# Kernel tuning notes

Hardware: AMD Instinct MI355X
Metric: run time of the kernel (lower is better)

Reference implementation:

```python
import jax, jax.numpy as jnp
import numpy as np

EPS = 1e-5
ABIT = 8
WBIT = 8


def ste_round(x):
    # straight-through rounding (HAWQ SymmetricQuantFunction)
    return x + jax.lax.stop_gradient(jnp.round(x) - x)


def quant_act(x, bit=ABIT):
    # per-tensor symmetric activation quantization (QuantAct)
    n = 2.0 ** (bit - 1) - 1  # 127
    scale = jnp.max(jnp.abs(x)) / n
    x_int = jnp.clip(ste_round(x / scale), -n - 1, n)
    return x_int * scale, scale


def setup_inputs() -> dict:
    key = jax.random.key(0)
    k = jax.random.split(key, 6)
    B, C_in, H, W, C_out = 32, 512, 32, 32, 128
    x = jax.random.normal(k[0], (B, C_in, H, W), jnp.float32)
    # incoming activation scale (input assumed already 8-bit quantized)
    act_scaling_factor = (jnp.max(jnp.abs(x)) / 127.0).reshape(1)
    bn_gamma = jax.random.uniform(k[1], (C_in,), jnp.float32, 0.5, 1.5)
    bn_beta = jax.random.normal(k[2], (C_in,), jnp.float32) * 0.1
    bn_mean = jax.random.normal(k[3], (C_in,), jnp.float32) * 0.1
    bn_var = jax.random.uniform(k[4], (C_in,), jnp.float32, 0.5, 1.5)
    conv_weight = jax.random.normal(k[5], (C_out, C_in, 3, 3), jnp.float32) / np.sqrt(C_in * 9)
    return {"x": x, "act_scaling_factor": act_scaling_factor,
            "bn_gamma": bn_gamma, "bn_beta": bn_beta,
            "bn_mean": bn_mean, "bn_var": bn_var,
            "conv_weight": conv_weight}


def reference(x, act_scaling_factor, bn_gamma, bn_beta, bn_mean, bn_var, conv_weight):
    nw = 2.0 ** (WBIT - 1) - 1  # 127
    s_in = act_scaling_factor.reshape(())

    # ---- QuantBn: fold BN into per-channel affine, quantize weight/bias ----
    w_bn = bn_gamma / jnp.sqrt(bn_var + EPS)            # [C_in]
    b_bn = bn_beta - bn_mean * w_bn                      # [C_in]
    ws_bn = jnp.max(jnp.abs(w_bn)) / nw                  # per-tensor weight scale
    w_int = jnp.clip(ste_round(w_bn / ws_bn), -nw - 1, nw)
    bn_sf = ws_bn * s_in                                 # bn output scaling factor
    b_int = ste_round(b_bn / bn_sf)
    x_int = x / s_in
    x = (x_int * w_int[None, :, None, None] + b_int[None, :, None, None]) * bn_sf

    # ---- ReLU ----
    x = jax.nn.relu(x)

    # ---- QuantAct: requantize activations to 8 bit ----
    x, s_act = quant_act(x)

    # ---- QuantConv2d: per-output-channel 8-bit weight quant, int conv ----
    ws_c = jnp.max(jnp.abs(conv_weight), axis=(1, 2, 3)) / nw       # [C_out]
    w_cint = jnp.clip(ste_round(conv_weight / ws_c[:, None, None, None]), -nw - 1, nw)
    y_int = jax.lax.conv_general_dilated(
        x / s_act, w_cint, window_strides=(1, 1), padding=((1, 1), (1, 1)),
        dimension_numbers=("NCHW", "OIHW", "NCHW"))
    conv_sf = s_act * ws_c                               # [C_out]
    y = y_int * conv_sf[None, :, None, None]

    # ---- QuantAct output requant ----
    y, s_out = quant_act(y)
    return (y, s_out)
```

## Files before the change

### kernel.cpp

```cpp
#include <hip/hip_runtime.h>


typedef int v4i __attribute__((ext_vector_type(4)));

#define WS_A1    64
#define WS_B1    2112
#define WS_WSC   4160
#define WS_XMX   4672
#define WS_XMN   6720
#define WS_WQ    8768
#define WS_X2    598592
#define WS_ZROW  18424384

__device__ __forceinline__ float wave_max(float m) {
#pragma unroll
    for (int off = 32; off; off >>= 1) m = fmaxf(m, __shfl_xor(m, off));
    return m;
}

__device__ __forceinline__ void stage16(const char* g, char* s, int lane) {
#if defined(__has_builtin) && __has_builtin(__builtin_amdgcn_global_load_lds)
    __builtin_amdgcn_global_load_lds(
        (const __attribute__((address_space(1))) void*)g,
        (__attribute__((address_space(3))) void*)s, 16, 0, 0);
#else
    *(v4i*)(s + lane * 16) = *(const v4i*)g;
#endif
}

__global__ __launch_bounds__(512) void k_prep(
    const float* __restrict__ gamma, const float* __restrict__ beta,
    const float* __restrict__ mean,  const float* __restrict__ var,
    const float* __restrict__ asf,   const float* __restrict__ cw,
    const float4* __restrict__ x4,
    float* ws_f, unsigned* ws_u, float* __restrict__ wsc,
    signed char* __restrict__ wq) {
    int t = threadIdx.x;
    int bid = blockIdx.x;
    __shared__ float red[16];
    if (bid < 512) {
        int c = bid;
        float mx = -3.4e38f, mn = 3.4e38f;
#pragma unroll
        for (int r = 0; r < 16; ++r) {
            int bbb = r * 2 + (t >> 8);
            float4 v = x4[((size_t)(bbb * 512 + c)) * 256 + (t & 255)];
            mx = fmaxf(mx, fmaxf(fmaxf(v.x, v.y), fmaxf(v.z, v.w)));
            mn = fminf(mn, fminf(fminf(v.x, v.y), fminf(v.z, v.w)));
        }
        mx = wave_max(mx);
        mn = -wave_max(-mn);
        if ((t & 63) == 0) { red[t >> 6] = mx; red[8 + (t >> 6)] = mn; }
        __syncthreads();
        if (t == 0) {
            float M = red[0], N = red[8];
#pragma unroll
            for (int i = 1; i < 8; ++i) { M = fmaxf(M, red[i]); N = fminf(N, red[8 + i]); }
            ws_f[WS_XMX / 4 + c] = M;
            ws_f[WS_XMN / 4 + c] = N;
        }
    } else if (bid < 640) {
        int co = bid - 512;
        const float* w = cw + (size_t)co * 4608;
        float m = 0.f;
        for (int j = t; j < 4608; j += 512) m = fmaxf(m, fabsf(w[j]));
        m = wave_max(m);
        if ((t & 63) == 0) red[t >> 6] = m;
        __syncthreads();
        float mall = red[0];
#pragma unroll
        for (int i = 1; i < 8; ++i) mall = fmaxf(mall, red[i]);
        float sc = mall / 127.0f;
        if (t == 0) wsc[co] = sc;
        int ci = t >> 6, cq = (t >> 4) & 3, cb = t & 15;
#pragma unroll
        for (int tap = 0; tap < 9; ++tap) {
            float q = fminf(fmaxf(rintf(w[t * 9 + tap] / sc), -128.f), 127.f);
            wq[(((size_t)(tap * 8 + ci) * 4 + cq) * 128 + co) * 16 + cb] = (signed char)q;
        }
    } else {
        float wbn = gamma[t] / sqrtf(var[t] + 1e-5f);
        float bbn = beta[t] - mean[t] * wbn;
        float m = wave_max(fabsf(wbn));
        if ((t & 63) == 0) red[t >> 6] = m;
        __syncthreads();
        float mall = red[0];
#pragma unroll
        for (int i = 1; i < 8; ++i) mall = fmaxf(mall, red[i]);
        float ws_bn = mall / 127.0f;
        float s_in  = asf[0];
        float bn_sf = ws_bn * s_in;
        float wint  = fminf(fmaxf(rintf(wbn / ws_bn), -128.f), 127.f);
        float bint  = rintf(bbn / bn_sf);
        ws_f[WS_A1 / 4 + t] = wint * bn_sf / s_in;
        ws_f[WS_B1 / 4 + t] = bint * bn_sf;
        if (t == 0) ws_u[1] = 0u;
    }
}

__global__ __launch_bounds__(256) void k_xquant(
    const float4* __restrict__ x4, float* __restrict__ ws_f,
    unsigned* __restrict__ x2u, unsigned* __restrict__ zrowu) {
    int bb = 31 - (blockIdx.x >> 5), h = blockIdx.x & 31;
    const float* A1 = ws_f + WS_A1 / 4;
    const float* B1 = ws_f + WS_B1 / 4;
    const float* XMX = ws_f + WS_XMX / 4;
    const float* XMN = ws_f + WS_XMN / 4;
    int t = threadIdx.x;

    __shared__ float sred[4];
    float cand = 0.f;
#pragma unroll
    for (int c0 = 0; c0 < 512; c0 += 256) {
        int c = c0 + t;
        float A = A1[c], B = B1[c];
        cand = fmaxf(cand, fmaxf(fmaf(XMX[c], A, B), fmaf(XMN[c], A, B)));
    }
    cand = wave_max(cand);
    if ((t & 63) == 0) sred[t >> 6] = cand;
    __syncthreads();
    float xm = fmaxf(fmaxf(sred[0], sred[1]), fmaxf(sred[2], sred[3]));
    float inv_sact = 127.0f / xm;
    if (blockIdx.x == 0 && t == 0) ws_f[3] = xm / 127.0f;

    size_t rowd = (size_t)(bb * 32 + h) * 4352;
    {
        int p = t >> 3, side = (t >> 2) & 1, d = t & 3;
        x2u[rowd + (p * 34 + side * 33) * 4 + d] = 0u;
    }
    if (blockIdx.x < 17) {
        int idx = blockIdx.x * 256 + t;
        if (idx < 4352) zrowu[idx] = 0u;
    }

    __shared__ unsigned lds[512 * 9];

#pragma unroll
    for (int it = 0; it < 16; ++it) {
        int idx = it * 256 + t;
        int c = idx >> 3, f4 = idx & 7;
        float4 v = x4[((size_t)bb * 512 + c) * 256 + h * 8 + f4];
        float A = A1[c] * inv_sact, B = B1[c] * inv_sact;
        unsigned q0 = (unsigned)(int)fminf(rintf(fmaxf(fmaf(v.x, A, B), 0.f)), 127.f);
        unsigned q1 = (unsigned)(int)fminf(rintf(fmaxf(fmaf(v.y, A, B), 0.f)), 127.f);
        unsigned q2 = (unsigned)(int)fminf(rintf(fmaxf(fmaf(v.z, A, B), 0.f)), 127.f);
        unsigned q3 = (unsigned)(int)fminf(rintf(fmaxf(fmaf(v.w, A, B), 0.f)), 127.f);
        lds[c * 9 + f4] = q0 | (q1 << 8) | (q2 << 16) | (q3 << 24);
    }
    __syncthreads();

#pragma unroll
    for (int it = 0; it < 4; ++it) {
        int p = it * 8 + (t >> 5);
        int s = (t >> 2) & 7;
        int k = t & 3;
        unsigned L[16];
#pragma unroll
        for (int j = 0; j < 16; ++j) L[j] = lds[(p * 16 + j) * 9 + s];
        uint4 o;
        unsigned* op = (unsigned*)&o;
#pragma unroll
        for (int d = 0; d < 4; ++d)
            op[d] = ((L[4 * d] >> (8 * k)) & 255u) |
                    (((L[4 * d + 1] >> (8 * k)) & 255u) << 8) |
                    (((L[4 * d + 2] >> (8 * k)) & 255u) << 16) |
                    (((L[4 * d + 3] >> (8 * k)) & 255u) << 24);
        *(uint4*)(x2u + rowd + (size_t)(p * 34 + s * 4 + 1 + k) * 4) = o;
    }
}

__global__ __launch_bounds__(256, 2) void k_conv(
    const unsigned char* __restrict__ x2, const unsigned char* __restrict__ zrow,
    const signed char* __restrict__ wq,
    const float* __restrict__ wsc, const float* __restrict__ ws_f,
    unsigned* __restrict__ amaxy, float* __restrict__ y) {
    __shared__ char ldsb[73728];
    int t = threadIdx.x;
    int lane = t & 63, wv = t >> 6;
    int kv = wv & 1, rp = wv >> 1;
    int m = lane & 15, quad = lane >> 4;

    int bid = blockIdx.x;
    int tile = (bid & 7) * 64 + (bid >> 3);
    int ch = tile & 1;
    int rg = (tile >> 1) & 7;
    int bb = tile >> 4;
    int co0 = ch * 64;
    int h0 = rg * 4 + rp * 2;

    const unsigned char* xb = x2 + (size_t)bb * (32 * 17408);
    const v4i* rpt[4];
#pragma unroll
    for (int j = 0; j < 4; ++j) {
        int row = h0 - 1 + j;
        rpt[j] = (const v4i*)(((unsigned)row < 32u) ? (xb + (size_t)row * 17408) : zrow);
    }

    v4i acc[4][4];
#pragma unroll
    for (int i = 0; i < 4; ++i)
#pragma unroll
        for (int j = 0; j < 4; ++j) acc[i][j] = (v4i){0, 0, 0, 0};

    int abase = quad * 34 + m;

    for (int j = 0; j < 4; ++j) {
#pragma unroll
        for (int i = 0; i < 18; ++i) {
            int c = wv * 18 + i;
            int kvs = (c >= 36) ? 1 : 0;
            int rem = c - kvs * 36;
            int tap = rem >> 2, cq = rem & 3;
            int ci = kvs * 4 + j;
            const char* g = (const char*)wq +
                ((((size_t)(tap * 8 + ci) * 4 + cq) * 128 + co0) * 16) + lane * 16;
            char* s = ldsb + (((kvs * 9 + tap) * 4 + cq) << 10);
            stage16(g, s, lane);
        }
        __syncthreads();

        int ci = kv * 4 + j;
        const v4i* bbase = (const v4i*)ldsb + kv * 2304;
#pragma unroll
        for (int kh = 0; kh < 3; ++kh)
#pragma unroll
            for (int kw = 0; kw < 3; ++kw) {
                int tap = kh * 3 + kw;
                v4i a[4];
#pragma unroll
                for (int mt = 0; mt < 4; ++mt)
                    a[mt] = rpt[kh + (mt >> 1)][ci * 136 + abase + kw + (mt & 1) * 16];
#pragma unroll
                for (int nt = 0; nt < 4; ++nt) {
                    v4i bf = bbase[(tap * 4 + quad) * 64 + nt * 16 + m];
#pragma unroll
                    for (int mt = 0; mt < 4; ++mt)
                        acc[mt][nt] = __builtin_amdgcn_mfma_i32_16x16x64_i8(a[mt], bf, acc[mt][nt], 0, 0, 0);
                }
            }
        __syncthreads();
    }

    v4i* red = (v4i*)ldsb;
    if (kv == 1) {
#pragma unroll
        for (int mt = 0; mt < 4; ++mt)
#pragma unroll
            for (int nt = 0; nt < 4; ++nt)
                red[((rp * 16 + mt * 4 + nt) << 6) + lane] = acc[mt][nt];
    }
    __syncthreads();
    if (kv == 0) {
#pragma unroll
        for (int mt = 0; mt < 4; ++mt)
#pragma unroll
            for (int nt = 0; nt < 4; ++nt) {
                v4i p = red[((rp * 16 + mt * 4 + nt) << 6) + lane];
                acc[mt][nt].x += p.x; acc[mt][nt].y += p.y;
                acc[mt][nt].z += p.z; acc[mt][nt].w += p.w;
            }

        float s_act = ws_f[3];
        float mx = 0.f;
#pragma unroll
        for (int nt = 0; nt < 4; ++nt) {
            int co = co0 + nt * 16 + m;
            float sf = s_act * wsc[co];
#pragma unroll
            for (int mt = 0; mt < 4; ++mt) {
                int row = h0 + (mt >> 1);
                float* yb = y + ((size_t)(bb * 128 + co)) * 1024 + row * 32 + (mt & 1) * 16;
                float4 vv;
                vv.x = (float)acc[mt][nt][0] * sf;
                vv.y = (float)acc[mt][nt][1] * sf;
                vv.z = (float)acc[mt][nt][2] * sf;
                vv.w = (float)acc[mt][nt][3] * sf;
                *(float4*)(yb + quad * 4) = vv;
                mx = fmaxf(mx, fmaxf(fmaxf(fabsf(vv.x), fabsf(vv.y)),
                                     fmaxf(fabsf(vv.z), fabsf(vv.w))));
            }
        }
        mx = wave_max(mx);
        if (lane == 0) atomicMax(amaxy, __float_as_uint(mx));
    }
}

__global__ __launch_bounds__(256) void k_yquant(float* __restrict__ yout,
                                                const unsigned* __restrict__ ws_u) {
    float s_out = __uint_as_float(ws_u[1]) / 127.0f;
    float4* y4 = (float4*)yout;
    int stride = gridDim.x * blockDim.x;
    for (int i = blockIdx.x * blockDim.x + threadIdx.x; i < 1048576; i += stride) {
        float4 v = y4[i];
        v.x = fminf(fmaxf(rintf(v.x / s_out), -128.f), 127.f) * s_out;
        v.y = fminf(fmaxf(rintf(v.y / s_out), -128.f), 127.f) * s_out;
        v.z = fminf(fmaxf(rintf(v.z / s_out), -128.f), 127.f) * s_out;
        v.w = fminf(fmaxf(rintf(v.w / s_out), -128.f), 127.f) * s_out;
        y4[i] = v;
    }
    if (blockIdx.x == 0 && threadIdx.x == 0) yout[4194304] = s_out;
}

extern "C" void kernel_launch(void* const* d_in, const int* in_sizes, int n_in,
                              void* d_out, int out_size, void* d_ws, size_t ws_size,
                              hipStream_t stream) {
    const float* x     = (const float*)d_in[0];
    const float* asf   = (const float*)d_in[1];
    const float* gamma = (const float*)d_in[2];
    const float* beta  = (const float*)d_in[3];
    const float* mean  = (const float*)d_in[4];
    const float* var   = (const float*)d_in[5];
    const float* cw    = (const float*)d_in[6];

    float*    ws_f = (float*)d_ws;
    unsigned* ws_u = (unsigned*)d_ws;
    signed char*   wq   = (signed char*)d_ws + WS_WQ;
    unsigned char* x2   = (unsigned char*)d_ws + WS_X2;
    unsigned char* zrow = (unsigned char*)d_ws + WS_ZROW;
    float* y = (float*)d_out;

    k_prep<<<641, 512, 0, stream>>>(gamma, beta, mean, var, asf, cw,
                                    (const float4*)x, ws_f, ws_u,
                                    ws_f + WS_WSC / 4, wq);
    k_xquant<<<1024, 256, 0, stream>>>((const float4*)x, ws_f,
                                       (unsigned*)x2, (unsigned*)zrow);
    k_conv<<<512, 256, 0, stream>>>(x2, zrow, wq, ws_f + WS_WSC / 4,
                                    ws_f, ws_u + 1, y);
    k_yquant<<<1024, 256, 0, stream>>>(y, ws_u);
}
```

Measured before the change: 160.2 us.

## Switch conv to 32x32x32 int8 MFMA with halved weight staging and higher occupancy

The int8 conv kernel moves from 16x16x64 MFMA tiles to 32x32x32 tiles. The quantized weight layout changes to match, and per-stage weight staging is halved by iterating over 8 channel chunks instead of 4, so LDS per block drops enough to allow 4 blocks per CU. A-fragment loads are reused across the three kh taps, which cuts global/L2 reads of activation rows. The trade-off is more K-loop iterations with more barriers, plus higher register pressure from the 16-wide accumulators under the tighter launch bound.

```diff
diff --git a/kernel.cpp b/kernel.cpp
--- a/kernel.cpp
+++ b/kernel.cpp
@@ -1,7 +1,8 @@
 #include <hip/hip_runtime.h>
 
 
-typedef int v4i __attribute__((ext_vector_type(4)));
+typedef int v4i  __attribute__((ext_vector_type(4)));
+typedef int v16i __attribute__((ext_vector_type(16)));
 
 #define WS_A1    64
 #define WS_B1    2112
@@ -72,11 +73,11 @@
         for (int i = 1; i < 8; ++i) mall = fmaxf(mall, red[i]);
         float sc = mall / 127.0f;
         if (t == 0) wsc[co] = sc;
-        int ci = t >> 6, cq = (t >> 4) & 3, cb = t & 15;
+        int cdw = t >> 4, cb = t & 15;
 #pragma unroll
         for (int tap = 0; tap < 9; ++tap) {
             float q = fminf(fmaxf(rintf(w[t * 9 + tap] / sc), -128.f), 127.f);
-            wq[(((size_t)(tap * 8 + ci) * 4 + cq) * 128 + co) * 16 + cb] = (signed char)q;
+            wq[(((size_t)tap * 32 + cdw) * 128 + co) * 16 + cb] = (signed char)q;
         }
     } else {
         float wbn = gamma[t] / sqrtf(var[t] + 1e-5f);
@@ -169,16 +170,16 @@
     }
 }
 
-__global__ __launch_bounds__(256, 2) void k_conv(
+__global__ __launch_bounds__(256, 4) void k_conv(
     const unsigned char* __restrict__ x2, const unsigned char* __restrict__ zrow,
     const signed char* __restrict__ wq,
     const float* __restrict__ wsc, const float* __restrict__ ws_f,
     unsigned* __restrict__ amaxy, float* __restrict__ y) {
-    __shared__ char ldsb[73728];
+    __shared__ char ldsb[36864];
     int t = threadIdx.x;
     int lane = t & 63, wv = t >> 6;
     int kv = wv & 1, rp = wv >> 1;
-    int m = lane & 15, quad = lane >> 4;
+    int m = lane & 31, khalf = lane >> 5;
 
     int bid = blockIdx.x;
     int tile = (bid & 7) * 64 + (bid >> 3);
@@ -189,95 +190,96 @@
     int h0 = rg * 4 + rp * 2;
 
     const unsigned char* xb = x2 + (size_t)bb * (32 * 17408);
-    const v4i* rpt[4];
+    const char* rpt[4];
 #pragma unroll
     for (int j = 0; j < 4; ++j) {
         int row = h0 - 1 + j;
-        rpt[j] = (const v4i*)(((unsigned)row < 32u) ? (xb + (size_t)row * 17408) : zrow);
-    }
-
-    v4i acc[4][4];
-#pragma unroll
-    for (int i = 0; i < 4; ++i)
-#pragma unroll
-        for (int j = 0; j < 4; ++j) acc[i][j] = (v4i){0, 0, 0, 0};
-
-    int abase = quad * 34 + m;
-
-    for (int j = 0; j < 4; ++j) {
-#pragma unroll
-        for (int i = 0; i < 18; ++i) {
-            int c = wv * 18 + i;
-            int kvs = (c >= 36) ? 1 : 0;
-            int rem = c - kvs * 36;
-            int tap = rem >> 2, cq = rem & 3;
-            int ci = kvs * 4 + j;
+        rpt[j] = (const char*)(((unsigned)row < 32u) ? (xb + (size_t)row * 17408) : zrow);
+    }
+
+    v16i acc[2][2];
+#pragma unroll
+    for (int i = 0; i < 2; ++i)
+#pragma unroll
+        for (int j = 0; j < 2; ++j)
+#pragma unroll
+            for (int e = 0; e < 16; ++e) acc[i][j][e] = 0;
+
+    for (int j = 0; j < 8; ++j) {
+#pragma unroll
+        for (int i = 0; i < 9; ++i) {
+            int c = wv * 9 + i;
+            int s = (c >= 18) ? 1 : 0;
+            int r = c - s * 18;
+            int tap = r >> 1, kh = r & 1;
+            int ci = s * 8 + j;
             const char* g = (const char*)wq +
-                ((((size_t)(tap * 8 + ci) * 4 + cq) * 128 + co0) * 16) + lane * 16;
-            char* s = ldsb + (((kvs * 9 + tap) * 4 + cq) << 10);
-            stage16(g, s, lane);
-        }
-        __syncthreads();
-
-        int ci = kv * 4 + j;
-        const v4i* bbase = (const v4i*)ldsb + kv * 2304;
-#pragma unroll
-        for (int kh = 0; kh < 3; ++kh)
-#pragma unroll
-            for (int kw = 0; kw < 3; ++kw) {
+                (((size_t)(tap * 32 + ci * 2 + kh) * 128 + co0) * 16) + lane * 16;
+            char* sdst = ldsb + s * 18432 + (tap * 2 + kh) * 1024;
+            stage16(g, sdst, lane);
+        }
+        __syncthreads();
+
+        int ci = kv * 8 + j;
+        const char* bslot = ldsb + kv * 18432;
+        int aoff = (ci * 2 + khalf) * 544 + m * 16;
+#pragma unroll
+        for (int kw = 0; kw < 3; ++kw) {
+            v4i a[4];
+#pragma unroll
+            for (int r = 0; r < 4; ++r)
+                a[r] = *(const v4i*)(rpt[r] + aoff + kw * 16);
+#pragma unroll
+            for (int kh = 0; kh < 3; ++kh) {
                 int tap = kh * 3 + kw;
-                v4i a[4];
-#pragma unroll
-                for (int mt = 0; mt < 4; ++mt)
-                    a[mt] = rpt[kh + (mt >> 1)][ci * 136 + abase + kw + (mt & 1) * 16];
-#pragma unroll
-                for (int nt = 0; nt < 4; ++nt) {
-                    v4i bf = bbase[(tap * 4 + quad) * 64 + nt * 16 + m];
-#pragma unroll
-                    for (int mt = 0; mt < 4; ++mt)
-                        acc[mt][nt] = __builtin_amdgcn_mfma_i32_16x16x64_i8(a[mt], bf, acc[mt][nt], 0, 0, 0);
+#pragma unroll
+                for (int nt = 0; nt < 2; ++nt) {
+                    v4i bf = *(const v4i*)(bslot + (tap * 2 + khalf) * 1024 + (nt * 32 + m) * 16);
+                    acc[0][nt] = __builtin_amdgcn_mfma_i32_32x32x32_i8(a[kh], bf, acc[0][nt], 0, 0, 0);
+                    acc[1][nt] = __builtin_amdgcn_mfma_i32_32x32x32_i8(a[kh + 1], bf, acc[1][nt], 0, 0, 0);
                 }
             }
+        }
         __syncthreads();
     }
 
     v4i* red = (v4i*)ldsb;
     if (kv == 1) {
 #pragma unroll
-        for (int mt = 0; mt < 4; ++mt)
-#pragma unroll
-            for (int nt = 0; nt < 4; ++nt)
-                red[((rp * 16 + mt * 4 + nt) << 6) + lane] = acc[mt][nt];
+        for (int mt = 0; mt < 2; ++mt)
+#pragma unroll
+            for (int nt = 0; nt < 2; ++nt) {
+                const int* ap = (const int*)&acc[mt][nt];
+#pragma unroll
+                for (int g = 0; g < 4; ++g)
+                    red[((((rp * 2 + mt) * 2 + nt) * 4 + g) << 6) + lane] = *(const v4i*)(ap + 4 * g);
+            }
     }
     __syncthreads();
     if (kv == 0) {
-#pragma unroll
-        for (int mt = 0; mt < 4; ++mt)
-#pragma unroll
-            for (int nt = 0; nt < 4; ++nt) {
-                v4i p = red[((rp * 16 + mt * 4 + nt) << 6) + lane];
-                acc[mt][nt].x += p.x; acc[mt][nt].y += p.y;
-                acc[mt][nt].z += p.z; acc[mt][nt].w += p.w;
-            }
-
         float s_act = ws_f[3];
         float mx = 0.f;
 #pragma unroll
-        for (int nt = 0; nt < 4; ++nt) {
-            int co = co0 + nt * 16 + m;
-            float sf = s_act * wsc[co];
-#pragma unroll
-            for (int mt = 0; mt < 4; ++mt) {
-                int row = h0 + (mt >> 1);
-                float* yb = y + ((size_t)(bb * 128 + co)) * 1024 + row * 32 + (mt & 1) * 16;
-                float4 vv;
-                vv.x = (float)acc[mt][nt][0] * sf;
-                vv.y = (float)acc[mt][nt][1] * sf;
-                vv.z = (float)acc[mt][nt][2] * sf;
-                vv.w = (float)acc[mt][nt][3] * sf;
-                *(float4*)(yb + quad * 4) = vv;
-                mx = fmaxf(mx, fmaxf(fmaxf(fabsf(vv.x), fabsf(vv.y)),
-                                     fmaxf(fabsf(vv.z), fabsf(vv.w))));
+        for (int mt = 0; mt < 2; ++mt) {
+            int row = h0 + mt;
+#pragma unroll
+            for (int nt = 0; nt < 2; ++nt) {
+                int* ap = (int*)&acc[mt][nt];
+                int co = co0 + nt * 32 + m;
+                float sf = s_act * wsc[co];
+                float* yb = y + ((size_t)(bb * 128 + co)) * 1024 + row * 32 + khalf * 4;
+#pragma unroll
+                for (int g = 0; g < 4; ++g) {
+                    v4i p = red[((((rp * 2 + mt) * 2 + nt) * 4 + g) << 6) + lane];
+                    float4 vv;
+                    vv.x = (float)(ap[4 * g + 0] + p.x) * sf;
+                    vv.y = (float)(ap[4 * g + 1] + p.y) * sf;
+                    vv.z = (float)(ap[4 * g + 2] + p.z) * sf;
+                    vv.w = (float)(ap[4 * g + 3] + p.w) * sf;
+                    *(float4*)(yb + 8 * g) = vv;
+                    mx = fmaxf(mx, fmaxf(fmaxf(fabsf(vv.x), fabsf(vv.y)),
+                                         fmaxf(fabsf(vv.z), fabsf(vv.w))));
+                }
             }
         }
         mx = wave_max(mx);
```

Result: slower. 165.6 us (+3.4%).
